# Optimization experiments

Measured on AMD Instinct MI355X. Metric: run time of the kernel, lower is better.

The kernel has to match this reference:

```python
import jax, jax.numpy as jnp
import numpy as np

K = 3          # kernel_size
STRIDE = 1
PAD = 1
DIL = 1
K2 = K * K


def conv2d(x, w, b):
    # standard NCHW conv matching nn.Conv2d(stride, padding, dilation)
    y = jax.lax.conv_general_dilated(
        x, w, window_strides=(STRIDE, STRIDE),
        padding=[(PAD, PAD), (PAD, PAD)], rhs_dilation=(DIL, DIL),
        dimension_numbers=('NCHW', 'OIHW', 'NCHW'))
    return y + b[None, :, None, None]


def setup_inputs() -> dict:
    key = jax.random.key(0)
    ks = jax.random.split(key, 7)
    B, C, H, W, O = 4, 64, 128, 128, 64
    x = jax.random.normal(ks[0], (B, C, H, W), jnp.float32)
    weight = jax.random.normal(ks[1], (O, C, K, K), jnp.float32) * 0.05
    bias = jax.random.normal(ks[2], (O,), jnp.float32) * 0.05
    # offset/modulation convs (small weights so sample points stay near grid)
    offset_w = jax.random.normal(ks[3], (2 * K2, C, K, K), jnp.float32) * 0.01
    offset_b = jax.random.normal(ks[4], (2 * K2,), jnp.float32) * 0.1
    mod_w = jax.random.normal(ks[5], (K2, C, K, K), jnp.float32) * 0.01
    mod_b = jnp.ones((K2,), jnp.float32)  # torch init: modulation bias = 1
    return dict(x=x, weight=weight, bias=bias, offset_w=offset_w,
                offset_b=offset_b, mod_w=mod_w, mod_b=mod_b)


def _forward(x, weight, bias, offset_w, offset_b, mod_w, mod_b):
    B, C, H, W = x.shape
    O = weight.shape[0]
    offsets = conv2d(x, offset_w, offset_b)              # (B, 2*K2, Ho, Wo)
    mod = jax.nn.sigmoid(conv2d(x, mod_w, mod_b))        # (B, K2, Ho, Wo)
    Ho, Wo = offsets.shape[2], offsets.shape[3]
    off = offsets.reshape(B, 2, K2, Ho, Wo)
    # base sampling position: single center per output pixel (as in source)
    base_y = jnp.arange(Ho, dtype=x.dtype) * STRIDE - PAD + (K // 2) * DIL
    base_x = jnp.arange(Wo, dtype=x.dtype) * STRIDE - PAD + (K // 2) * DIL
    sy = base_y[None, None, :, None] + off[:, 0]         # (B, K2, Ho, Wo)
    sx = base_x[None, None, None, :] + off[:, 1]
    # bilinear sampling, zero padding, align_corners=True semantics
    y0 = jnp.floor(sy)
    x0 = jnp.floor(sx)
    wy1 = sy - y0
    wx1 = sx - x0
    y0i = y0.astype(jnp.int32)
    x0i = x0.astype(jnp.int32)
    P = K2 * Ho * Wo
    xf = x.reshape(B, C, H * W)

    def gather(yi, xi):
        valid = ((yi >= 0) & (yi < H) & (xi >= 0) & (xi < W))
        lin = (jnp.clip(yi, 0, H - 1) * W + jnp.clip(xi, 0, W - 1)).reshape(B, P)
        g = jax.vmap(lambda xb, lb: xb[:, lb])(xf, lin)   # (B, C, P)
        return g * valid.reshape(B, 1, P).astype(x.dtype)

    wy1f = wy1.reshape(B, 1, P)
    wx1f = wx1.reshape(B, 1, P)
    g00 = gather(y0i, x0i)
    g01 = gather(y0i, x0i + 1)
    g10 = gather(y0i + 1, x0i)
    g11 = gather(y0i + 1, x0i + 1)
    sampled = ((1.0 - wy1f) * ((1.0 - wx1f) * g00 + wx1f * g01)
               + wy1f * ((1.0 - wx1f) * g10 + wx1f * g11))
    sampled = sampled.reshape(B, C, K2, Ho * Wo)
    wk = weight.reshape(O, C, K2)
    out = jnp.einsum('bckp,ock->bop', sampled, wk).reshape(B, O, Ho, Wo)
    out = out * mod.mean(axis=1, keepdims=True) + bias[None, :, None, None]
    return out


def reference(x, weight, bias, offset_w, offset_b, mod_w, mod_b):
    return _forward(x, weight, bias, offset_w, offset_b, mod_w, mod_b)
```

## Files before the change

### kernel.cpp

```cpp
#include <hip/hip_runtime.h>
#include <math.h>

namespace {

constexpr int B = 4, C = 64, O = 64, H = 128, W = 128, K2 = 9;
constexpr int HW = H * W;
constexpr int PIX = 128;
constexpr int STR = 64;
constexpr int WROWS = 4, WCOLS = STR + 3, WCELLS = WROWS * WCOLS;

typedef __attribute__((ext_vector_type(8))) short short8v;
typedef __attribute__((ext_vector_type(4))) float f32x4;
typedef __attribute__((ext_vector_type(2))) float f32x2;
typedef __attribute__((ext_vector_type(4))) unsigned u32x4;

__device__ __forceinline__ unsigned f2bf(float f) {
    unsigned u = __float_as_uint(f);
    return (u + 0x7FFFu + ((u >> 16) & 1u)) >> 16;
}
__device__ __forceinline__ unsigned cvtpk(float lo, float hi) {
    unsigned r;
    asm("v_cvt_pk_bf16_f32 %0, %1, %2" : "=v"(r) : "v"(lo), "v"(hi));
    return r;
}
__device__ __forceinline__ f32x2 up2(unsigned d) {
    f32x2 r;
    r[0] = __uint_as_float(d << 16);
    r[1] = __uint_as_float(d & 0xffff0000u);
    return r;
}
__device__ __forceinline__ int swz(int r, int off) {
    return (r << 7) + (off ^ ((r & 7) << 4));
}

constexpr size_t WSW_OFF = 0;
constexpr size_t WSA_OFF = 73728;
constexpr size_t WS_NEED = 110592;

__global__ void k0_pack(const float* __restrict__ w, const float* __restrict__ ow,
                        const float* __restrict__ mw, unsigned char* __restrict__ ws)
{
    const int id = blockIdx.x * 256 + threadIdx.x;
    if (id < 4608) {
        const int k = id >> 9, rem = id & 511, ks = rem >> 8, r2 = rem & 255;
        const int ot = r2 >> 6, lane = r2 & 63;
        const int o = ot * 16 + (lane & 15), cb = ks * 32 + (lane >> 4) * 8;
        unsigned pk[4];
        #pragma unroll
        for (int e = 0; e < 4; ++e)
            pk[e] = f2bf(w[(o * C + cb + 2 * e) * 9 + k])
                  | (f2bf(w[(o * C + cb + 2 * e + 1) * 9 + k]) << 16);
        *(uint4*)(ws + WSW_OFF + (size_t)id * 16) = make_uint4(pk[0], pk[1], pk[2], pk[3]);
    } else if (id < 6912) {
        const int id2 = id - 4608;
        const int k = id2 >> 8, rem = id2 & 255, ks = rem >> 7, r2 = rem & 127;
        const int mt = r2 >> 6, lane = r2 & 63;
        const int r = mt * 16 + (lane & 15), cb = ks * 32 + (lane >> 4) * 8;
        unsigned pk[4];
        #pragma unroll
        for (int e = 0; e < 4; ++e) {
            float v0 = 0.f, v1 = 0.f;
            const int c0 = cb + 2 * e;
            if (r < 18)      { v0 = ow[(r * C + c0) * 9 + k];        v1 = ow[(r * C + c0 + 1) * 9 + k]; }
            else if (r < 27) { v0 = mw[((r - 18) * C + c0) * 9 + k]; v1 = mw[((r - 18) * C + c0 + 1) * 9 + k]; }
            pk[e] = f2bf(v0) | (f2bf(v1) << 16);
        }
        *(uint4*)(ws + WSA_OFF + (size_t)id2 * 16) = make_uint4(pk[0], pk[1], pk[2], pk[3]);
    }
}

__global__ __launch_bounds__(256, 4)
void dcn_fused11(const float* __restrict__ x, const float* __restrict__ bias,
                 const float* __restrict__ ob, const float* __restrict__ mb,
                 const unsigned char* __restrict__ ws, float* __restrict__ out)
{
    __shared__ __align__(16) unsigned char sW[WCELLS * 128];
    __shared__ float offL[18 * STR];

    const int tid = threadIdx.x;
    const int lane = tid & 63, wv = tid >> 6;
    const int lrow = lane & 15, lk = lane >> 4;

    const int raw = blockIdx.x;
    const int bid = (raw & 7) * 128 + (raw >> 3);
    const int b = bid >> 8;
    const int s = bid & 255;
    const int ho = s >> 1;
    const int wo0 = (s & 1) * STR;

    const float* __restrict__ xb = x + b * C * HW;

    for (int t = tid; t < 2 * WCELLS; t += 256) {
        const int cell = t >> 1, chalf = t & 1;
        const int row = cell / WCOLS, col = cell - row * WCOLS;
        const int y = ho - 1 + row, xg = wo0 - 2 + col;
        const bool v = (y >= 0) & (y < H) & (xg >= 0) & (xg < W);
        const float vf = v ? 1.f : 0.f;
        const float* __restrict__ xp = xb + (v ? (y * W + xg) : 0);
        #pragma unroll
        for (int q = 0; q < 4; ++q) {
            unsigned pk[4];
            #pragma unroll
            for (int e = 0; e < 4; ++e) {
                const int c0 = chalf * 32 + q * 8 + 2 * e;
                pk[e] = cvtpk(vf * xp[c0 * HW], vf * xp[(c0 + 1) * HW]);
            }
            *(uint4*)(sW + swz(cell, chalf * 64 + q * 16)) = make_uint4(pk[0], pk[1], pk[2], pk[3]);
        }
    }
    __syncthreads();

    f32x4 oacc[2];
    #pragma unroll
    for (int mt = 0; mt < 2; ++mt)
        #pragma unroll
        for (int j = 0; j < 4; ++j) oacc[mt][j] = 0.f;

    #pragma unroll
    for (int k = 0; k < 9; ++k) {
        const int ky = k / 3, kx = k - ky * 3;
        const int cellb = ky * WCOLS + (wv * 16 + lrow) + kx + 1;
        #pragma unroll
        for (int ks = 0; ks < 2; ++ks) {
            short8v bf = *(const short8v*)(sW + swz(cellb, ks * 64 + lk * 16));
            #pragma unroll
            for (int mt = 0; mt < 2; ++mt) {
                short8v af = *(const short8v*)(ws + WSA_OFF +
                    (size_t)((((k * 2 + ks) * 2 + mt) * 64 + lane)) * 16);
                oacc[mt] = __builtin_amdgcn_mfma_f32_16x16x32_bf16(af, bf, oacc[mt], 0, 0, 0);
            }
        }
    }

    float mpart = 0.f;
    {
        const int pc = wv * 16 + lrow;
        #pragma unroll
        for (int mt = 0; mt < 2; ++mt) {
            #pragma unroll
            for (int j = 0; j < 4; ++j) {
                const int r = mt * 16 + lk * 4 + j;
                const float val = oacc[mt][j];
                if (r < 9)       offL[r * STR + pc] = (float)ho + ob[r] + val;
                else if (r < 18) offL[r * STR + pc] = (float)(wo0 + pc) + ob[r] + val;
                else if (r < 27) mpart += 1.f / (1.f + __expf(-(val + mb[r - 18])));
            }
        }
    }
    mpart += __shfl_xor(mpart, 16);
    mpart += __shfl_xor(mpart, 32);
    const float mm = mpart * (1.f / 9.f);
    __syncthreads();

    const int px = wv * 16 + lrow;

    f32x4 acc[4];
    #pragma unroll
    for (int ot = 0; ot < 4; ++ot)
        #pragma unroll
        for (int j = 0; j < 4; ++j) acc[ot][j] = 0.f;

    #pragma unroll 3
    for (int k = 0; k < 9; ++k) {
        const float syv = offL[k * STR + px];
        const float sxv = offL[(9 + k) * STR + px];
        const float fy = floorf(syv), fx = floorf(sxv);
        const float wy1 = syv - fy, wx1 = sxv - fx;
        const float wy0 = 1.f - wy1, wx0 = 1.f - wx1;
        const int y0 = (int)fy, x0 = (int)fx;
        const int rw = y0 - (ho - 1), cw = x0 - (wo0 - 2);
        const bool inw = (rw >= 0) & (rw <= WROWS - 2) & (cw >= 0) & (cw <= WCOLS - 2);
        const float u00 = wy0 * wx0, u01 = wy0 * wx1;
        const float u10 = wy1 * wx0, u11 = wy1 * wx1;

        short8v bfrag[2];
        if (__builtin_expect(inw, 1)) {
            const int c00 = rw * WCOLS + cw;
            #pragma unroll
            for (int ks = 0; ks < 2; ++ks) {
                const int chOff = ks * 64 + lk * 16;
                const uint4 d00 = *(const uint4*)(sW + swz(c00,             chOff));
                const uint4 d01 = *(const uint4*)(sW + swz(c00 + 1,         chOff));
                const uint4 d10 = *(const uint4*)(sW + swz(c00 + WCOLS,     chOff));
                const uint4 d11 = *(const uint4*)(sW + swz(c00 + WCOLS + 1, chOff));
                auto bil = [&](unsigned a, unsigned bb, unsigned c, unsigned d) -> unsigned {
                    f32x2 sacc = up2(a);
                    sacc *= u00;
                    sacc += up2(bb) * u01;
                    sacc += up2(c)  * u10;
                    sacc += up2(d)  * u11;
                    return cvtpk(sacc[0], sacc[1]);
                };
                u32x4 wvv;
                wvv[0] = bil(d00.x, d01.x, d10.x, d11.x);
                wvv[1] = bil(d00.y, d01.y, d10.y, d11.y);
                wvv[2] = bil(d00.z, d01.z, d10.z, d11.z);
                wvv[3] = bil(d00.w, d01.w, d10.w, d11.w);
                bfrag[ks] = __builtin_bit_cast(short8v, wvv);
            }
        } else {
            const float vy0 = (y0 >= 0 && y0 < H) ? 1.f : 0.f;
            const float vy1 = (y0 + 1 >= 0 && y0 + 1 < H) ? 1.f : 0.f;
            const float vx0 = (x0 >= 0 && x0 < W) ? 1.f : 0.f;
            const float vx1 = (x0 + 1 >= 0 && x0 + 1 < W) ? 1.f : 0.f;
            const int cy0 = min(max(y0, 0), H - 1), cy1 = min(max(y0 + 1, 0), H - 1);
            const int cx0 = min(max(x0, 0), W - 1), cx1 = min(max(x0 + 1, 0), W - 1);
            const int l00 = cy0 * W + cx0, l01 = cy0 * W + cx1;
            const int l10 = cy1 * W + cx0, l11 = cy1 * W + cx1;
            const float g00 = u00 * vy0 * vx0, g01 = u01 * vy0 * vx1;
            const float g10 = u10 * vy1 * vx0, g11 = u11 * vy1 * vx1;
            #pragma unroll
            for (int ks = 0; ks < 2; ++ks) {
                #pragma unroll
                for (int j = 0; j < 8; ++j) {
                    const float* __restrict__ xc = xb + (ks * 32 + lk * 8 + j) * HW;
                    const float sv = g00 * xc[l00] + g01 * xc[l01]
                                   + g10 * xc[l10] + g11 * xc[l11];
                    bfrag[ks][j] = (short)f2bf(sv);
                }
            }
        }

        #pragma unroll
        for (int ks = 0; ks < 2; ++ks) {
            #pragma unroll
            for (int ot = 0; ot < 4; ++ot) {
                short8v af = *(const short8v*)(ws + WSW_OFF +
                    (size_t)(((k * 8 + ks * 4 + ot) * 64 + lane)) * 16);
                acc[ot] = __builtin_amdgcn_mfma_f32_16x16x32_bf16(af, bfrag[ks], acc[ot], 0, 0, 0);
            }
        }
    }

    #pragma unroll
    for (int ot = 0; ot < 4; ++ot) {
        #pragma unroll
        for (int j = 0; j < 4; ++j) {
            const int o = ot * 16 + lk * 4 + j;
            out[(b * O + o) * HW + ho * W + wo0 + px] = acc[ot][j] * mm + bias[o];
        }
    }
}

__global__ __launch_bounds__(256, 2)
void dcn_fallback(const float* __restrict__ x, const float* __restrict__ weight,
                  const float* __restrict__ bias, const float* __restrict__ ow,
                  const float* __restrict__ ob, const float* __restrict__ mw,
                  const float* __restrict__ mb, float* __restrict__ out)
{
    __shared__ __align__(16) unsigned char sT[PIX * 128];
    __shared__ float offL[32 * PIX];
    __shared__ float mmL[PIX];

    const int tid = threadIdx.x;
    const int lane = tid & 63;
    const int wv = tid >> 6;
    const int bid = (blockIdx.x & 7) * 64 + (blockIdx.x >> 3);
    const int b = bid >> 7;
    const int ho = bid & 127;
    const float* __restrict__ xb = x + (size_t)b * C * HW;
    const int p = tid & 127, half = tid >> 7, wo = p;
    const int lrow = lane & 15, lk = lane >> 4;

    f32x4 oacc[2][2];
    #pragma unroll
    for (int mt = 0; mt < 2; ++mt)
        #pragma unroll
        for (int nt = 0; nt < 2; ++nt)
            #pragma unroll
            for (int j = 0; j < 4; ++j) oacc[mt][nt][j] = 0.0f;

    #pragma unroll
    for (int k = 0; k < K2; ++k) {
        const int ky = k / 3, kx = k % 3;
        short8v afrA[2][2];
        #pragma unroll
        for (int ks = 0; ks < 2; ++ks)
            #pragma unroll
            for (int mt = 0; mt < 2; ++mt) {
                const int r = mt * 16 + lrow, cb = ks * 32 + lk * 8;
                #pragma unroll
                for (int j = 0; j < 8; ++j) {
                    float wvv = 0.0f;
                    if (r < 18)      wvv = ow[((size_t)(r * C + cb + j)) * 9 + k];
                    else if (r < 27) wvv = mw[((size_t)((r - 18) * C + cb + j)) * 9 + k];
                    afrA[ks][mt][j] = (short)f2bf(wvv);
                }
            }
        {
            const int y = ho - 1 + ky, xx = wo - 1 + kx;
            const bool v = (y >= 0) & (y < H) & (xx >= 0) & (xx < W);
            const float vf = v ? 1.0f : 0.0f;
            const float* __restrict__ xp = xb + (v ? (y * W + xx) : 0);
            #pragma unroll
            for (int q = 0; q < 4; ++q) {
                unsigned pk[4];
                #pragma unroll
                for (int e = 0; e < 4; ++e) {
                    const int c0 = half * 32 + q * 8 + e * 2;
                    pk[e] = f2bf(vf * xp[(size_t)c0 * HW]) | (f2bf(vf * xp[(size_t)(c0 + 1) * HW]) << 16);
                }
                *(uint4*)(sT + swz(p, half * 64 + q * 16)) = make_uint4(pk[0], pk[1], pk[2], pk[3]);
            }
        }
        __syncthreads();
        #pragma unroll
        for (int ks = 0; ks < 2; ++ks)
            #pragma unroll
            for (int nt = 0; nt < 2; ++nt) {
                const int pc = wv * 32 + nt * 16 + lrow;
                short8v bfr = *(const short8v*)(sT + swz(pc, ks * 64 + lk * 16));
                #pragma unroll
                for (int mt = 0; mt < 2; ++mt)
                    oacc[mt][nt] = __builtin_amdgcn_mfma_f32_16x16x32_bf16(afrA[ks][mt], bfr, oacc[mt][nt], 0, 0, 0);
            }
        __syncthreads();
    }

    #pragma unroll
    for (int mt = 0; mt < 2; ++mt)
        #pragma unroll
        for (int nt = 0; nt < 2; ++nt)
            #pragma unroll
            for (int j = 0; j < 4; ++j) {
                const int r = mt * 16 + lk * 4 + j;
                const int pc = wv * 32 + nt * 16 + lrow;
                float bv = 0.0f;
                if (r < 18)      bv = ob[r];
                else if (r < 27) bv = mb[r - 18];
                offL[r * PIX + pc] = oacc[mt][nt][j] + bv;
            }
    __syncthreads();

    float sy[K2], sx[K2];
    #pragma unroll
    for (int k = 0; k < K2; ++k) {
        sy[k] = (float)ho + offL[k * PIX + p];
        sx[k] = (float)wo + offL[(9 + k) * PIX + p];
    }
    if (half == 0) {
        float mm = 0.0f;
        #pragma unroll
        for (int k = 0; k < K2; ++k)
            mm += 1.0f / (1.0f + __expf(-offL[(18 + k) * PIX + p]));
        mmL[p] = mm * (1.0f / 9.0f);
    }

    f32x4 acc[8];
    #pragma unroll
    for (int nt = 0; nt < 8; ++nt)
        #pragma unroll
        for (int j = 0; j < 4; ++j) acc[nt][j] = 0.0f;

    #pragma unroll
    for (int k = 0; k < K2; ++k) {
        short8v afr[2];
        #pragma unroll
        for (int ks = 0; ks < 2; ++ks) {
            const int o = wv * 16 + lrow, cb = ks * 32 + lk * 8;
            #pragma unroll
            for (int j = 0; j < 8; ++j)
                afr[ks][j] = (short)f2bf(weight[((size_t)(o * C + cb + j)) * 9 + k]);
        }
        {
            const float fy = floorf(sy[k]), fx = floorf(sx[k]);
            const float wy1 = sy[k] - fy, wx1 = sx[k] - fx;
            const float wy0 = 1.0f - wy1, wx0 = 1.0f - wx1;
            const int y0 = (int)fy, x0 = (int)fx, y1 = y0 + 1, x1 = x0 + 1;
            const float vy0 = (y0 >= 0 && y0 < H) ? 1.0f : 0.0f;
            const float vy1 = (y1 >= 0 && y1 < H) ? 1.0f : 0.0f;
            const float vx0 = (x0 >= 0 && x0 < W) ? 1.0f : 0.0f;
            const float vx1 = (x1 >= 0 && x1 < W) ? 1.0f : 0.0f;
            const int cy0 = min(max(y0, 0), H - 1), cy1 = min(max(y1, 0), H - 1);
            const int cx0 = min(max(x0, 0), W - 1), cx1 = min(max(x1, 0), W - 1);
            const int l00 = cy0 * W + cx0, l01 = cy0 * W + cx1;
            const int l10 = cy1 * W + cx0, l11 = cy1 * W + cx1;
            const float w00 = wy0 * wx0 * vy0 * vx0, w01 = wy0 * wx1 * vy0 * vx1;
            const float w10 = wy1 * wx0 * vy1 * vx0, w11 = wy1 * wx1 * vy1 * vx1;
            #pragma unroll
            for (int q = 0; q < 4; ++q) {
                unsigned pk[4];
                #pragma unroll
                for (int e = 0; e < 4; ++e) {
                    const int c0 = half * 32 + q * 8 + e * 2;
                    const float* __restrict__ xc0 = xb + (size_t)c0 * HW;
                    const float* __restrict__ xc1 = xc0 + HW;
                    const float s0 = w00 * xc0[l00] + w01 * xc0[l01] + w10 * xc0[l10] + w11 * xc0[l11];
                    const float s1 = w00 * xc1[l00] + w01 * xc1[l01] + w10 * xc1[l10] + w11 * xc1[l11];
                    pk[e] = f2bf(s0) | (f2bf(s1) << 16);
                }
                *(uint4*)(sT + swz(p, half * 64 + q * 16)) = make_uint4(pk[0], pk[1], pk[2], pk[3]);
            }
        }
        __syncthreads();
        #pragma unroll
        for (int ks = 0; ks < 2; ++ks)
            #pragma unroll
            for (int nt = 0; nt < 8; ++nt) {
                const int pc = nt * 16 + lrow;
                short8v bfr = *(const short8v*)(sT + swz(pc, ks * 64 + lk * 16));
                acc[nt] = __builtin_amdgcn_mfma_f32_16x16x32_bf16(afr[ks], bfr, acc[nt], 0, 0, 0);
            }
        __syncthreads();
    }

    float bv[4];
    #pragma unroll
    for (int j = 0; j < 4; ++j) bv[j] = bias[wv * 16 + lk * 4 + j];
    #pragma unroll
    for (int nt = 0; nt < 8; ++nt) {
        const int pc = nt * 16 + lrow;
        const float mmv = mmL[pc];
        #pragma unroll
        for (int j = 0; j < 4; ++j) {
            const int o = wv * 16 + lk * 4 + j;
            out[((size_t)(b * O + o)) * HW + ho * W + pc] = acc[nt][j] * mmv + bv[j];
        }
    }
}

}

extern "C" void kernel_launch(void* const* d_in, const int* in_sizes, int n_in,
                              void* d_out, int out_size, void* d_ws, size_t ws_size,
                              hipStream_t stream)
{
    const float* x  = (const float*)d_in[0];
    const float* w  = (const float*)d_in[1];
    const float* bs = (const float*)d_in[2];
    const float* ow = (const float*)d_in[3];
    const float* ob = (const float*)d_in[4];
    const float* mw = (const float*)d_in[5];
    const float* mb = (const float*)d_in[6];
    float* out = (float*)d_out;

    if (ws_size < WS_NEED) {
        dim3 grid(B * H), block(256);
        hipLaunchKernelGGL(dcn_fallback, grid, block, 0, stream,
                           x, w, bs, ow, ob, mw, mb, out);
        return;
    }

    unsigned char* ws = (unsigned char*)d_ws;
    hipLaunchKernelGGL(k0_pack, dim3(27), dim3(256), 0, stream, w, ow, mw, ws);
    hipLaunchKernelGGL(dcn_fused11, dim3(1024), dim3(256), 0, stream,
                       x, bs, ob, mb, (const unsigned char*)ws, out);
}
```

Baseline: 42.69 us.

## Halve pixel strip per block and split deform taps across wave pairs

Each block now covers 32 output pixels instead of 64, so twice as many blocks launch and occupancy is raised to 8 blocks per CU. Within a block, the offset conv work is split across the four waves by M and N tile, and the nine deformable taps are divided between two wave pairs (5 and 4 taps). The partial accumulators are then reduced through shared memory before the output is written. This is meant to increase parallelism and latency hiding, at the cost of a larger halo overhead per pixel (67 columns for 64 pixels becomes 35 for 32), an extra LDS reduction with two more barriers, and an uneven tap split.

```diff
diff --git a/kernel.cpp b/kernel.cpp
--- a/kernel.cpp
+++ b/kernel.cpp
@@ -6,7 +6,7 @@
 constexpr int B = 4, C = 64, O = 64, H = 128, W = 128, K2 = 9;
 constexpr int HW = H * W;
 constexpr int PIX = 128;
-constexpr int STR = 64;
+constexpr int STR = 32;
 constexpr int WROWS = 4, WCOLS = STR + 3, WCELLS = WROWS * WCOLS;
 
 typedef __attribute__((ext_vector_type(8))) short short8v;
@@ -69,8 +69,8 @@
     }
 }
 
-__global__ __launch_bounds__(256, 4)
-void dcn_fused11(const float* __restrict__ x, const float* __restrict__ bias,
+__global__ __launch_bounds__(256, 8)
+void dcn_fused12(const float* __restrict__ x, const float* __restrict__ bias,
                  const float* __restrict__ ob, const float* __restrict__ mb,
                  const unsigned char* __restrict__ ws, float* __restrict__ out)
 {
@@ -82,11 +82,11 @@
     const int lrow = lane & 15, lk = lane >> 4;
 
     const int raw = blockIdx.x;
-    const int bid = (raw & 7) * 128 + (raw >> 3);
-    const int b = bid >> 8;
-    const int s = bid & 255;
-    const int ho = s >> 1;
-    const int wo0 = (s & 1) * STR;
+    const int bid = (raw & 7) * 256 + (raw >> 3);
+    const int b = bid >> 9;
+    const int s = bid & 511;
+    const int ho = s >> 2;
+    const int wo0 = (s & 3) * STR;
 
     const float* __restrict__ xb = x + b * C * HW;
 
@@ -110,41 +110,34 @@
     }
     __syncthreads();
 
-    f32x4 oacc[2];
-    #pragma unroll
-    for (int mt = 0; mt < 2; ++mt)
-        #pragma unroll
-        for (int j = 0; j < 4; ++j) oacc[mt][j] = 0.f;
+    const int mtA = wv >> 1, ntA = wv & 1;
+    f32x4 oacc;
+    #pragma unroll
+    for (int j = 0; j < 4; ++j) oacc[j] = 0.f;
 
     #pragma unroll
     for (int k = 0; k < 9; ++k) {
         const int ky = k / 3, kx = k - ky * 3;
-        const int cellb = ky * WCOLS + (wv * 16 + lrow) + kx + 1;
+        const int cellb = ky * WCOLS + (ntA * 16 + lrow) + kx + 1;
         #pragma unroll
         for (int ks = 0; ks < 2; ++ks) {
             short8v bf = *(const short8v*)(sW + swz(cellb, ks * 64 + lk * 16));
-            #pragma unroll
-            for (int mt = 0; mt < 2; ++mt) {
-                short8v af = *(const short8v*)(ws + WSA_OFF +
-                    (size_t)((((k * 2 + ks) * 2 + mt) * 64 + lane)) * 16);
-                oacc[mt] = __builtin_amdgcn_mfma_f32_16x16x32_bf16(af, bf, oacc[mt], 0, 0, 0);
-            }
+            short8v af = *(const short8v*)(ws + WSA_OFF +
+                (size_t)((((k * 2 + ks) * 2 + mtA) * 64 + lane)) * 16);
+            oacc = __builtin_amdgcn_mfma_f32_16x16x32_bf16(af, bf, oacc, 0, 0, 0);
         }
     }
 
     float mpart = 0.f;
     {
-        const int pc = wv * 16 + lrow;
-        #pragma unroll
-        for (int mt = 0; mt < 2; ++mt) {
-            #pragma unroll
-            for (int j = 0; j < 4; ++j) {
-                const int r = mt * 16 + lk * 4 + j;
-                const float val = oacc[mt][j];
-                if (r < 9)       offL[r * STR + pc] = (float)ho + ob[r] + val;
-                else if (r < 18) offL[r * STR + pc] = (float)(wo0 + pc) + ob[r] + val;
-                else if (r < 27) mpart += 1.f / (1.f + __expf(-(val + mb[r - 18])));
-            }
+        const int pc = ntA * 16 + lrow;
+        #pragma unroll
+        for (int j = 0; j < 4; ++j) {
+            const int r = mtA * 16 + lk * 4 + j;
+            const float val = oacc[j];
+            if (r < 9)       offL[r * STR + pc] = (float)ho + ob[r] + val;
+            else if (r < 18) offL[r * STR + pc] = (float)(wo0 + pc) + ob[r] + val;
+            else if (r < 27) mpart += 1.f / (1.f + __expf(-(val + mb[r - 18])));
         }
     }
     mpart += __shfl_xor(mpart, 16);
@@ -152,7 +145,7 @@
     const float mm = mpart * (1.f / 9.f);
     __syncthreads();
 
-    const int px = wv * 16 + lrow;
+    const int px = (wv & 1) * 16 + lrow;
 
     f32x4 acc[4];
     #pragma unroll
@@ -160,8 +153,7 @@
         #pragma unroll
         for (int j = 0; j < 4; ++j) acc[ot][j] = 0.f;
 
-    #pragma unroll 3
-    for (int k = 0; k < 9; ++k) {
+    auto doTap = [&](int k) {
         const float syv = offL[k * STR + px];
         const float sxv = offL[(9 + k) * STR + px];
         const float fy = floorf(syv), fx = floorf(sxv);
@@ -230,14 +222,39 @@
                 acc[ot] = __builtin_amdgcn_mfma_f32_16x16x32_bf16(af, bfrag[ks], acc[ot], 0, 0, 0);
             }
         }
-    }
-
-    #pragma unroll
-    for (int ot = 0; ot < 4; ++ot) {
-        #pragma unroll
-        for (int j = 0; j < 4; ++j) {
-            const int o = ot * 16 + lk * 4 + j;
-            out[(b * O + o) * HW + ho * W + wo0 + px] = acc[ot][j] * mm + bias[o];
+    };
+
+    if (wv < 2) {
+        #pragma unroll
+        for (int k = 0; k < 5; ++k) doTap(k);
+    } else {
+        #pragma unroll
+        for (int k = 5; k < 9; ++k) doTap(k);
+    }
+
+    __syncthreads();
+    if (wv < 2) {
+        #pragma unroll
+        for (int ot = 0; ot < 4; ++ot) {
+            const int boff = ot * 64 + lk * 16;
+            *(f32x4*)(sW + (px << 8) + (boff ^ ((px & 7) << 4))) = acc[ot];
+        }
+    }
+    __syncthreads();
+    if (wv >= 2) {
+        #pragma unroll
+        for (int ot = 0; ot < 4; ++ot) {
+            const int boff = ot * 64 + lk * 16;
+            f32x4 p = *(const f32x4*)(sW + (px << 8) + (boff ^ ((px & 7) << 4)));
+            acc[ot] += p;
+        }
+        #pragma unroll
+        for (int ot = 0; ot < 4; ++ot) {
+            #pragma unroll
+            for (int j = 0; j < 4; ++j) {
+                const int o = ot * 16 + lk * 4 + j;
+                out[(b * O + o) * HW + ho * W + wo0 + px] = acc[ot][j] * mm + bias[o];
+            }
         }
     }
 }
@@ -443,6 +460,6 @@
 
     unsigned char* ws = (unsigned char*)d_ws;
     hipLaunchKernelGGL(k0_pack, dim3(27), dim3(256), 0, stream, w, ow, mw, ws);
-    hipLaunchKernelGGL(dcn_fused11, dim3(1024), dim3(256), 0, stream,
+    hipLaunchKernelGGL(dcn_fused12, dim3(2048), dim3(256), 0, stream,
                        x, bs, ob, mb, (const unsigned char*)ws, out);
 }
```

Result: slower. 61.13 us (+43.2%).
